# Kernel tuning notes

Hardware: AMD Instinct MI355X
Metric: run time of the kernel (lower is better)

Reference implementation:

```python
import jax, jax.numpy as jnp
import numpy as np

H, D, EF, NT, ET = 4, 32, 32, 4, 8
N, E = 100000, 1600000
NEG_SLOPE = 0.2


def setup_inputs() -> dict:
    key = jax.random.key(0)
    ks = jax.random.split(key, 11)
    return {
        "feat": jax.random.normal(ks[0], (N, H * D), jnp.float32),
        "fc": jax.random.normal(ks[1], (NT, H, D), jnp.float32) * 0.1,
        "edge_emb": jax.random.normal(ks[2], (ET, EF), jnp.float32),
        "W_e": jax.random.normal(ks[3], (H * EF, EF), jnp.float32) * 0.1,
        "attn_l": jax.random.normal(ks[4], (1, H, D), jnp.float32) * 0.1,
        "attn_r": jax.random.normal(ks[5], (1, H, D), jnp.float32) * 0.1,
        "attn_e": jax.random.normal(ks[6], (1, H, EF), jnp.float32) * 0.1,
        "node_types": jax.random.randint(ks[7], (N,), 0, NT, jnp.int32),
        "e_feat": jax.random.randint(ks[8], (E,), 0, ET, jnp.int32),
        "src": jax.random.randint(ks[9], (E,), 0, N, jnp.int32),
        "dst": jax.random.randint(ks[10], (E,), 0, N, jnp.int32),
    }


def reference(feat, fc, edge_emb, W_e, attn_l, attn_r, attn_e, node_types, e_feat, src, dst):
    n = feat.shape[0]
    h = feat.reshape(n, H, D)                      # [N,H,D] (h_src == h_dst)
    fs = h * fc[node_types]                        # per-node-type scaling, feat_src == feat_dst

    # edge-type embedding path: Embedding -> Linear(edge_feats, H*edge_feats) -> attn_e score
    emb = (edge_emb @ W_e.T).reshape(ET, H, EF)    # [ET,H,EF]
    ee = (emb * attn_e).sum(-1)[e_feat]            # [E,H]

    el = (fs * attn_l).sum(-1)                     # [N,H]
    er = (fs * attn_r).sum(-1)                     # [N,H]
    e = jax.nn.leaky_relu(el[src] + er[dst] + ee, NEG_SLOPE)  # [E,H]

    # edge_softmax: segment softmax over destination node
    m = jax.ops.segment_max(e, dst, num_segments=n)           # [N,H]
    ex = jnp.exp(e - m[dst])
    s = jax.ops.segment_sum(ex, dst, num_segments=n)          # [N,H]
    a = ex / s[dst]                                            # [E,H]

    # u_mul_e + sum aggregation
    msg = fs[src] * a[:, :, None]                              # [E,H,D]
    rst = jax.ops.segment_sum(msg, dst, num_segments=n)       # [N,H,D]

    rst = rst + h                                              # residual (Identity, in==out feats)
    return rst, a[:, :, None]
```

## Files before the change

### kernel.cpp

```cpp
#include <hip/hip_runtime.h>
#include <stdint.h>

namespace {
constexpr int kH = 4, kD = 32, kEF = 32, kNT = 4, kET = 8;
constexpr int kHD = kH * kD;
constexpr float kNegSlope = 0.2f;
constexpr int kBN = 128;
constexpr int kNB = (100000 + kBN - 1) / kBN;
constexpr int kHB = 512;
constexpr int kCap = 4096;
constexpr int kXP = 20;

using f32x2 = __attribute__((ext_vector_type(2))) float;
using f32x4 = __attribute__((ext_vector_type(4))) float;

__device__ __forceinline__ float lrelu(float x) { return x > 0.f ? x : kNegSlope * x; }

__global__ void __launch_bounds__(256) k_init(
    const float* __restrict__ feat, const float* __restrict__ fc,
    const float* __restrict__ edge_emb, const float* __restrict__ W_e,
    const float* __restrict__ attn_l, const float* __restrict__ attn_r,
    const float* __restrict__ attn_e, const int* __restrict__ node_types,
    const int* __restrict__ dst, const int* __restrict__ src,
    const int* __restrict__ e_feat, int* __restrict__ cursor,
    int2* __restrict__ tmp, float* __restrict__ el, float* __restrict__ er,
    uint8_t* __restrict__ fs, float* __restrict__ ee_tab, int N, int E) {
  __shared__ int h[kNB], r[kNB];
  int t = threadIdx.x;
  if (blockIdx.x < kHB) {
    for (int i = t; i < kNB; i += 256) h[i] = 0;
    __syncthreads();
    int per = (E + kHB - 1) / kHB;
    int e0 = blockIdx.x * per;
    int e1 = min(e0 + per, E);
    for (int i = e0 + t; i < e1; i += 256) atomicAdd(&h[dst[i] >> 7], 1);
    __syncthreads();
    for (int i = t; i < kNB; i += 256) {
      int c = h[i];
      r[i] = i * kCap + (c ? atomicAdd(&cursor[i], c) : 0);
    }
    __syncthreads();
    for (int i = e0 + t; i < e1; i += 256) {
      int d = dst[i];
      int b = d >> 7;
      int pos = atomicAdd(&r[b], 1);
      int2 v2 = {src[i] | (e_feat[i] << 17) | ((d & 127) << 20), i};
      tmp[pos] = v2;
    }
  }
  if (blockIdx.x == 0 && t < kET * kH) {
    int et = t / kH, hh = t % kH;
    float acc = 0.f;
    for (int f = 0; f < kEF; ++f) {
      const float* wrow = W_e + (hh * kEF + f) * kEF;
      const float* erow = edge_emb + et * kEF;
      float emb = 0.f;
      for (int k = 0; k < kEF; ++k) emb += erow[k] * wrow[k];
      acc += emb * attn_e[hh * kEF + f];
    }
    ee_tab[et * kH + hh] = acc;
  }
  int gid = blockIdx.x * blockDim.x + t;
  int node = gid >> 5;
  int lane = t & 31;
  if (node >= N) return;
  int nt = node_types[node];
  float4 f4 = *(const float4*)(feat + ((size_t)node << 7) + lane * 4);
  float4 c4 = *(const float4*)(fc + nt * kHD + lane * 4);
  float4 al = *(const float4*)(attn_l + lane * 4);
  float4 ar = *(const float4*)(attn_r + lane * 4);
  float fx = f4.x * c4.x, fy = f4.y * c4.y, fz = f4.z * c4.z, fw = f4.w * c4.w;
  int w = __builtin_amdgcn_cvt_pk_fp8_f32(fx, fy, 0, false);
  w = __builtin_amdgcn_cvt_pk_fp8_f32(fz, fw, w, true);
  *(int*)(fs + ((size_t)node << 7) + lane * 4) = w;
  float pl = fx * al.x + fy * al.y + fz * al.z + fw * al.w;
  float pr = fx * ar.x + fy * ar.y + fz * ar.z + fw * ar.w;
#pragma unroll
  for (int off = 1; off < 8; off <<= 1) {
    pl += __shfl_xor(pl, off);
    pr += __shfl_xor(pr, off);
  }
  if ((lane & 7) == 0) {
    int hh = lane >> 3;
    el[node * kH + hh] = pl;
    er[node * kH + hh] = pr;
  }
}

__global__ void __launch_bounds__(256) k_build(const int* __restrict__ cursor,
                                               const int2* __restrict__ tmp,
                                               int* __restrict__ ptr,
                                               int2* __restrict__ csr2, int N, int E) {
  __shared__ int fh[128], fb[128], sc[128];
  __shared__ int red[256];
  int b = blockIdx.x, t = threadIdx.x;
  int acc = 0;
  for (int i = t; i < b; i += 256) acc += cursor[i];
  red[t] = acc;
  __syncthreads();
  for (int off = 128; off > 0; off >>= 1) {
    if (t < off) red[t] += red[t + off];
    __syncthreads();
  }
  int s0 = red[0];
  int cnt = min(cursor[b], kCap);
  const int2* slab = tmp + (size_t)b * kCap;
  if (t < 128) fh[t] = 0;
  __syncthreads();
  for (int j = t; j < cnt; j += 256) atomicAdd(&fh[slab[j].x >> 20], 1);
  __syncthreads();
  if (t < 128) sc[t] = fh[t];
  __syncthreads();
  for (int off = 1; off < 128; off <<= 1) {
    int v = 0;
    if (t < 128 && t >= off) v = sc[t - off];
    __syncthreads();
    if (t < 128) sc[t] += v;
    __syncthreads();
  }
  if (t < 128) {
    fb[t] = sc[t] - fh[t];
    int d = (b << 7) + t;
    if (d < N) ptr[d] = s0 + fb[t];
    fh[t] = 0;
  }
  if (b == gridDim.x - 1 && t == 0) ptr[N] = E;
  __syncthreads();
  for (int j = t; j < cnt; j += 256) {
    int2 v = slab[j];
    int dl = v.x >> 20;
    int r = atomicAdd(&fh[dl], 1);
    int2 o = {v.x & 0xFFFFF, v.y};
    csr2[s0 + fb[dl] + r] = o;
  }
}

__global__ void __launch_bounds__(256) k_fused(
    const uint8_t* __restrict__ fs, const float* __restrict__ feat,
    const float* __restrict__ el, const float* __restrict__ er,
    const float* __restrict__ ee_tab, const int* __restrict__ ptr,
    const int2* __restrict__ csr2, float* __restrict__ rst,
    float* __restrict__ out_a, int N) {
  __shared__ float ee_sh[kET * kH];
  __shared__ __align__(16) float xp[4][64 * kXP];
  if (threadIdx.x < kET * kH) ee_sh[threadIdx.x] = ee_tab[threadIdx.x];
  __syncthreads();
  int lane = threadIdx.x & 63;
  int wid = threadIdx.x >> 6;
  int node = blockIdx.x * 4 + wid;
  if (node >= N) return;
  int start = ptr[node], end = ptr[node + 1];
  int deg = end - start;
  bool big = deg > 64;

  int g = lane >> 3;
  int q = lane & 7;
  int head = q >> 1;
  int qoff = q << 4;
  float er_h = er[(node << 2) + head];
  f32x2 f2 = *(const f32x2*)(feat + ((size_t)node << 7) + lane * 2);

  float* exb = &xp[wid][0];
  int* eidb = (int*)&xp[wid][1024];

  float sm = 0.f;
  f32x2 acc[8];
#pragma unroll
  for (int k = 0; k < 8; ++k) acc[k] = (f32x2){0.f, 0.f};

  int j = start + g;
  int2 pk0 = csr2[(j < end) ? j : 0];
  int2 pk1 = csr2[(j + 8 < end) ? j + 8 : 0];
  int s0 = pk0.x & 0x1FFFF;
  float elv0 = el[(s0 << 2) + head];
  int4 w0 = *(const int4*)(fs + ((size_t)s0 << 7) + qoff);
  float ee0 = ee_sh[((pk0.x >> 17) << 2) + head];
  int s1 = pk1.x & 0x1FFFF;
  float elv1 = el[(s1 << 2) + head];
  int4 w1 = *(const int4*)(fs + ((size_t)s1 << 7) + qoff);
  float ee1 = ee_sh[((pk1.x >> 17) << 2) + head];
  int2 pk2 = csr2[(j + 16 < end) ? j + 16 : 0];

  int le = g;
  while (j < end) {
    int s2 = pk2.x & 0x1FFFF;
    float elv2 = el[(s2 << 2) + head];
    int4 w2 = *(const int4*)(fs + ((size_t)s2 << 7) + qoff);
    float ee2 = ee_sh[((pk2.x >> 17) << 2) + head];
    int2 pk3 = csr2[(j + 24 < end) ? j + 24 : 0];
    float ex = __expf(lrelu(elv0 + er_h + ee0));
    sm += ex;
    if (!big) {
      if ((q & 1) == 0) exb[(le << 2) + head] = ex;
      if (q == 7) eidb[le] = pk0.y;
    }
    f32x2 ex2 = {ex, ex};
#pragma unroll
    for (int c = 0; c < 4; ++c) {
      int wc = c == 0 ? w0.x : c == 1 ? w0.y : c == 2 ? w0.z : w0.w;
      acc[2 * c + 0] += ex2 * __builtin_amdgcn_cvt_pk_f32_fp8(wc, false);
      acc[2 * c + 1] += ex2 * __builtin_amdgcn_cvt_pk_f32_fp8(wc, true);
    }
    elv0 = elv1; w0 = w1; ee0 = ee1; pk0 = pk1;
    elv1 = elv2; w1 = w2; ee1 = ee2; pk1 = pk2;
    pk2 = pk3;
    j += 8;
    le += 8;
  }

  sm += __shfl_xor(sm, 8);
  sm += __shfl_xor(sm, 16);
  sm += __shfl_xor(sm, 32);
  float rinv = sm > 0.f ? 1.f / sm : 0.f;
  float rv0 = __shfl(rinv, 0), rv1 = __shfl(rinv, 2);
  float rv2 = __shfl(rinv, 4), rv3 = __shfl(rinv, 6);

  if (!big) {
    asm volatile("s_waitcnt lgkmcnt(0)" ::: "memory");
    __builtin_amdgcn_sched_barrier(0);
    if (lane < deg) {
      float4 e4 = *(const float4*)(exb + (lane << 2));
      int eid = eidb[lane];
      f32x4 a = {e4.x * rv0, e4.y * rv1, e4.z * rv2, e4.w * rv3};
      __builtin_nontemporal_store(a, (f32x4*)(out_a + ((size_t)eid << 2)));
    }
    __builtin_amdgcn_sched_barrier(0);
  } else {
    for (int jj = start + g; jj < end; jj += 8) {
      int2 pk = csr2[jj];
      int ss = pk.x & 0x1FFFF;
      float e_h = lrelu(el[(ss << 2) + head] + er_h +
                        ee_sh[((pk.x >> 17) << 2) + head]);
      float ex = __expf(e_h);
      float exA = __shfl_down(ex, 2);
      float exB = __shfl_down(ex, 4);
      float exC = __shfl_down(ex, 6);
      if (q == 0) {
        f32x4 a = {ex * rv0, exA * rv1, exB * rv2, exC * rv3};
        __builtin_nontemporal_store(a, (f32x4*)(out_a + ((size_t)pk.y << 2)));
      }
    }
  }

  float* row = &xp[wid][lane * kXP];
#pragma unroll
  for (int c = 0; c < 4; ++c) {
    float4 v4 = {acc[2 * c].x, acc[2 * c].y, acc[2 * c + 1].x, acc[2 * c + 1].y};
    *(float4*)(row + c * 4) = v4;
  }
  asm volatile("s_waitcnt lgkmcnt(0)" ::: "memory");
  __builtin_amdgcn_sched_barrier(0);
  int qsrc = lane >> 3;
  int coff = (lane & 7) * 2;
  const float* base = &xp[wid][qsrc * kXP + coff];
  f32x2 v = {0.f, 0.f};
#pragma unroll
  for (int gg = 0; gg < 8; ++gg) v += *(const f32x2*)(base + gg * 8 * kXP);

  float rs = __shfl(rinv, (lane >> 4) << 1);
  f32x2 o = v * rs + f2;
  __builtin_nontemporal_store(o, (f32x2*)(rst + ((size_t)node << 7) + lane * 2));
}

}

extern "C" void kernel_launch(void* const* d_in, const int* in_sizes, int n_in,
                              void* d_out, int out_size, void* d_ws, size_t ws_size,
                              hipStream_t stream) {
  const float* feat = (const float*)d_in[0];
  const float* fc = (const float*)d_in[1];
  const float* edge_emb = (const float*)d_in[2];
  const float* W_e = (const float*)d_in[3];
  const float* attn_l = (const float*)d_in[4];
  const float* attn_r = (const float*)d_in[5];
  const float* attn_e = (const float*)d_in[6];
  const int* node_types = (const int*)d_in[7];
  const int* e_feat = (const int*)d_in[8];
  const int* src = (const int*)d_in[9];
  const int* dst = (const int*)d_in[10];
  int N = in_sizes[7];
  int E = in_sizes[8];

  char* ws = (char*)d_ws;
  size_t off = 0;
  auto alloc = [&](size_t bytes) -> void* {
    void* p = ws + off;
    off = (off + bytes + 255) & ~(size_t)255;
    return p;
  };
  float* ee_tab = (float*)alloc((size_t)kET * kH * sizeof(float));
  float* el = (float*)alloc((size_t)N * kH * sizeof(float));
  float* er = (float*)alloc((size_t)N * kH * sizeof(float));
  uint8_t* fs = (uint8_t*)alloc((size_t)N * kHD * sizeof(uint8_t));
  int* cursor = (int*)alloc((size_t)kNB * sizeof(int));
  int* ptr = (int*)alloc((size_t)(N + 1) * sizeof(int));
  int2* tmp = (int2*)alloc((size_t)kNB * kCap * sizeof(int2));
  int2* csr2 = (int2*)alloc((size_t)E * sizeof(int2));

  hipMemsetAsync(cursor, 0, (size_t)kNB * sizeof(int), stream);
  k_init<<<(N + 7) / 8, 256, 0, stream>>>(feat, fc, edge_emb, W_e, attn_l, attn_r,
                                          attn_e, node_types, dst, src, e_feat,
                                          cursor, tmp, el, er, fs, ee_tab, N, E);
  k_build<<<kNB, 256, 0, stream>>>(cursor, tmp, ptr, csr2, N, E);

  float* rst = (float*)d_out;
  float* out_a = (float*)d_out + (size_t)N * kHD;
  k_fused<<<(N + 3) / 4, 256, 0, stream>>>(fs, feat, el, er, ee_tab, ptr, csr2,
                                           rst, out_a, N);
}
```

Baseline: 278.6 us.

## Split packed CSR into separate source and edge-id arrays

The interleaved int2 CSR array becomes two int arrays: packed source/type indices and edge ids. The main loop now streams only the 4-byte source index, and edge ids are read from global memory only when the attention output is written, which removes the LDS staging of edge ids. The change also lowers the number of histogram/scatter blocks in the init kernel and pads the LDS transpose stride from 20 to 21, presumably to reduce bank conflicts. The risk is an extra strided global read of eids in the store phase, and the odd stride may break the 16-byte alignment the float4 LDS row writes rely on.

Result: slower. 389.3 us (+39.7%).

```diff
diff --git a/kernel.cpp b/kernel.cpp
--- a/kernel.cpp
+++ b/kernel.cpp
@@ -7,9 +7,9 @@
 constexpr float kNegSlope = 0.2f;
 constexpr int kBN = 128;
 constexpr int kNB = (100000 + kBN - 1) / kBN;
-constexpr int kHB = 512;
+constexpr int kHB = 128;
 constexpr int kCap = 4096;
-constexpr int kXP = 20;
+constexpr int kXP = 21;
 
 using f32x2 = __attribute__((ext_vector_type(2))) float;
 using f32x4 = __attribute__((ext_vector_type(4))) float;
@@ -90,7 +90,8 @@
 __global__ void __launch_bounds__(256) k_build(const int* __restrict__ cursor,
                                                const int2* __restrict__ tmp,
                                                int* __restrict__ ptr,
-                                               int2* __restrict__ csr2, int N, int E) {
+                                               int* __restrict__ csr,
+                                               int* __restrict__ eids, int N, int E) {
   __shared__ int fh[128], fb[128], sc[128];
   __shared__ int red[256];
   int b = blockIdx.x, t = threadIdx.x;
@@ -130,8 +131,9 @@
     int2 v = slab[j];
     int dl = v.x >> 20;
     int r = atomicAdd(&fh[dl], 1);
-    int2 o = {v.x & 0xFFFFF, v.y};
-    csr2[s0 + fb[dl] + r] = o;
+    int pos = s0 + fb[dl] + r;
+    csr[pos] = v.x & 0xFFFFF;
+    eids[pos] = v.y;
   }
 }
 
@@ -139,8 +141,8 @@
     const uint8_t* __restrict__ fs, const float* __restrict__ feat,
     const float* __restrict__ el, const float* __restrict__ er,
     const float* __restrict__ ee_tab, const int* __restrict__ ptr,
-    const int2* __restrict__ csr2, float* __restrict__ rst,
-    float* __restrict__ out_a, int N) {
+    const int* __restrict__ csr, const int* __restrict__ eids,
+    float* __restrict__ rst, float* __restrict__ out_a, int N) {
   __shared__ float ee_sh[kET * kH];
   __shared__ __align__(16) float xp[4][64 * kXP];
   if (threadIdx.x < kET * kH) ee_sh[threadIdx.x] = ee_tab[threadIdx.x];
@@ -161,7 +163,6 @@
   f32x2 f2 = *(const f32x2*)(feat + ((size_t)node << 7) + lane * 2);
 
   float* exb = &xp[wid][0];
-  int* eidb = (int*)&xp[wid][1024];
 
   float sm = 0.f;
   f32x2 acc[8];
@@ -169,31 +170,28 @@
   for (int k = 0; k < 8; ++k) acc[k] = (f32x2){0.f, 0.f};
 
   int j = start + g;
-  int2 pk0 = csr2[(j < end) ? j : 0];
-  int2 pk1 = csr2[(j + 8 < end) ? j + 8 : 0];
-  int s0 = pk0.x & 0x1FFFF;
+  int pk0 = csr[(j < end) ? j : 0];
+  int pk1 = csr[(j + 8 < end) ? j + 8 : 0];
+  int s0 = pk0 & 0x1FFFF;
   float elv0 = el[(s0 << 2) + head];
   int4 w0 = *(const int4*)(fs + ((size_t)s0 << 7) + qoff);
-  float ee0 = ee_sh[((pk0.x >> 17) << 2) + head];
-  int s1 = pk1.x & 0x1FFFF;
+  float ee0 = ee_sh[((pk0 >> 17) << 2) + head];
+  int s1 = pk1 & 0x1FFFF;
   float elv1 = el[(s1 << 2) + head];
   int4 w1 = *(const int4*)(fs + ((size_t)s1 << 7) + qoff);
-  float ee1 = ee_sh[((pk1.x >> 17) << 2) + head];
-  int2 pk2 = csr2[(j + 16 < end) ? j + 16 : 0];
+  float ee1 = ee_sh[((pk1 >> 17) << 2) + head];
+  int pk2 = csr[(j + 16 < end) ? j + 16 : 0];
 
   int le = g;
   while (j < end) {
-    int s2 = pk2.x & 0x1FFFF;
+    int s2 = pk2 & 0x1FFFF;
     float elv2 = el[(s2 << 2) + head];
     int4 w2 = *(const int4*)(fs + ((size_t)s2 << 7) + qoff);
-    float ee2 = ee_sh[((pk2.x >> 17) << 2) + head];
-    int2 pk3 = csr2[(j + 24 < end) ? j + 24 : 0];
+    float ee2 = ee_sh[((pk2 >> 17) << 2) + head];
+    int pk3 = csr[(j + 24 < end) ? j + 24 : 0];
     float ex = __expf(lrelu(elv0 + er_h + ee0));
     sm += ex;
-    if (!big) {
-      if ((q & 1) == 0) exb[(le << 2) + head] = ex;
-      if (q == 7) eidb[le] = pk0.y;
-    }
+    if (!big && (q & 1) == 0) exb[(le << 2) + head] = ex;
     f32x2 ex2 = {ex, ex};
 #pragma unroll
     for (int c = 0; c < 4; ++c) {
@@ -201,8 +199,8 @@
       acc[2 * c + 0] += ex2 * __builtin_amdgcn_cvt_pk_f32_fp8(wc, false);
       acc[2 * c + 1] += ex2 * __builtin_amdgcn_cvt_pk_f32_fp8(wc, true);
     }
-    elv0 = elv1; w0 = w1; ee0 = ee1; pk0 = pk1;
-    elv1 = elv2; w1 = w2; ee1 = ee2; pk1 = pk2;
+    elv0 = elv1; w0 = w1; ee0 = ee1;
+    elv1 = elv2; w1 = w2; ee1 = ee2;
     pk2 = pk3;
     j += 8;
     le += 8;
@@ -220,24 +218,25 @@
     __builtin_amdgcn_sched_barrier(0);
     if (lane < deg) {
       float4 e4 = *(const float4*)(exb + (lane << 2));
-      int eid = eidb[lane];
+      int eid = eids[start + lane];
       f32x4 a = {e4.x * rv0, e4.y * rv1, e4.z * rv2, e4.w * rv3};
       __builtin_nontemporal_store(a, (f32x4*)(out_a + ((size_t)eid << 2)));
     }
     __builtin_amdgcn_sched_barrier(0);
   } else {
     for (int jj = start + g; jj < end; jj += 8) {
-      int2 pk = csr2[jj];
-      int ss = pk.x & 0x1FFFF;
+      int pk = csr[jj];
+      int ss = pk & 0x1FFFF;
       float e_h = lrelu(el[(ss << 2) + head] + er_h +
-                        ee_sh[((pk.x >> 17) << 2) + head]);
+                        ee_sh[((pk >> 17) << 2) + head]);
       float ex = __expf(e_h);
       float exA = __shfl_down(ex, 2);
       float exB = __shfl_down(ex, 4);
       float exC = __shfl_down(ex, 6);
       if (q == 0) {
+        int eid = eids[jj];
         f32x4 a = {ex * rv0, exA * rv1, exB * rv2, exC * rv3};
-        __builtin_nontemporal_store(a, (f32x4*)(out_a + ((size_t)pk.y << 2)));
+        __builtin_nontemporal_store(a, (f32x4*)(out_a + ((size_t)eid << 2)));
       }
     }
   }
@@ -295,16 +294,17 @@
   int* cursor = (int*)alloc((size_t)kNB * sizeof(int));
   int* ptr = (int*)alloc((size_t)(N + 1) * sizeof(int));
   int2* tmp = (int2*)alloc((size_t)kNB * kCap * sizeof(int2));
-  int2* csr2 = (int2*)alloc((size_t)E * sizeof(int2));
+  int* csr = (int*)alloc((size_t)E * sizeof(int));
+  int* eids = (int*)alloc((size_t)E * sizeof(int));
 
   hipMemsetAsync(cursor, 0, (size_t)kNB * sizeof(int), stream);
   k_init<<<(N + 7) / 8, 256, 0, stream>>>(feat, fc, edge_emb, W_e, attn_l, attn_r,
                                           attn_e, node_types, dst, src, e_feat,
                                           cursor, tmp, el, er, fs, ee_tab, N, E);
-  k_build<<<kNB, 256, 0, stream>>>(cursor, tmp, ptr, csr2, N, E);
+  k_build<<<kNB, 256, 0, stream>>>(cursor, tmp, ptr, csr, eids, N, E);
 
   float* rst = (float*)d_out;
   float* out_a = (float*)d_out + (size_t)N * kHD;
-  k_fused<<<(N + 3) / 4, 256, 0, stream>>>(fs, feat, el, er, ee_tab, ptr, csr2,
-                                           rst, out_a, N);
-}
+  k_fused<<<(N + 3) / 4, 256, 0, stream>>>(fs, feat, el, er, ee_tab, ptr, csr,
+                                           eids, rst, out_a, N);
+}
```
